# Kernel optimization log

Measured on AMD Instinct MI355X. Metric: run time of the kernel, lower is better.

Reference implementation:

```python
import jax, jax.numpy as jnp
import numpy as np

NEG_SLOPE = 0.2  # PyG GATConv default negative_slope


def _gat_conv(x, src, dst, W, a_src, a_dst, bias, heads, concat):
    """PyG-style GATConv (eval mode, self-loops already appended to src/dst).
    x: [N, Fin], W: [Fin, heads*C], a_src/a_dst: [heads, C], bias matches output.
    """
    N = x.shape[0]
    C = W.shape[1] // heads
    xw = (x @ W).reshape(N, heads, C)                      # [N, H, C]
    alpha_s = jnp.sum(xw * a_src, axis=-1)                 # [N, H]
    alpha_d = jnp.sum(xw * a_dst, axis=-1)                 # [N, H]
    e = jax.nn.leaky_relu(alpha_s[src] + alpha_d[dst], NEG_SLOPE)  # [E, H]
    # softmax over incoming edges of each destination node (numerically stable)
    m = jax.ops.segment_max(e, dst, num_segments=N)        # [N, H]
    e = jnp.exp(e - m[dst])
    denom = jax.ops.segment_sum(e, dst, num_segments=N)    # [N, H]
    alpha = e / denom[dst]                                 # [E, H]
    out = jax.ops.segment_sum(alpha[:, :, None] * xw[src], dst, num_segments=N)  # [N, H, C]
    if concat:
        out = out.reshape(N, heads * C)
    else:
        out = out.mean(axis=1)
    return out + bias


def setup_inputs() -> dict:
    key = jax.random.key(0)
    ks = jax.random.split(key, 10)
    N, E, FIN, FOUT, H1, C1 = 100000, 1600000, 128, 16, 4, 8
    x = jax.random.normal(ks[0], (N, FIN), jnp.float32)
    edge_index = jax.random.randint(ks[1], (2, E), 0, N, dtype=jnp.int32)
    W1 = jax.random.normal(ks[2], (FIN, H1 * C1), jnp.float32) / np.sqrt(FIN)
    a1_src = jax.random.normal(ks[3], (H1, C1), jnp.float32) / np.sqrt(C1)
    a1_dst = jax.random.normal(ks[4], (H1, C1), jnp.float32) / np.sqrt(C1)
    b1 = jnp.zeros((H1 * C1,), jnp.float32)
    W2 = jax.random.normal(ks[5], (H1 * C1, FOUT), jnp.float32) / np.sqrt(H1 * C1)
    a2_src = jax.random.normal(ks[6], (1, FOUT), jnp.float32) / np.sqrt(FOUT)
    a2_dst = jax.random.normal(ks[7], (1, FOUT), jnp.float32) / np.sqrt(FOUT)
    b2 = jnp.zeros((FOUT,), jnp.float32)
    return {"x": x, "edge_index": edge_index, "W1": W1, "a1_src": a1_src,
            "a1_dst": a1_dst, "b1": b1, "W2": W2, "a2_src": a2_src,
            "a2_dst": a2_dst, "b2": b2}


def reference(x, edge_index, W1, a1_src, a1_dst, b1, W2, a2_src, a2_dst, b2):
    N = x.shape[0]
    # PyG GATConv add_self_loops=True default
    loop = jnp.arange(N, dtype=edge_index.dtype)
    src = jnp.concatenate([edge_index[0], loop])
    dst = jnp.concatenate([edge_index[1], loop])
    # eval mode: F.dropout is identity
    h = _gat_conv(x, src, dst, W1, a1_src, a1_dst, b1, heads=4, concat=True)
    h = jax.nn.elu(h)
    h = _gat_conv(h, src, dst, W2, a2_src, a2_dst, b2, heads=1, concat=True)
    return jax.nn.log_softmax(h, axis=1)
```

## Files before the change

### kernel.cpp

```cpp
#include <hip/hip_runtime.h>
#include <math.h>

#define NN 100000
#define NE 1600000
#define ET (NE + NN)
#define FIN 128
#define H1 4
#define C1 8
#define F1 32
#define FOUT 16
#define NSLOPE 0.2f

#define PARTW 256
#define PSHIFT 8
#define NPART ((NN + PARTW - 1) / PARTW)
#define CHUNK 8192
#define NBLK ((ET + CHUNK - 1) / CHUNK)
#define CPAD 16
#define SMASK 0x1FFFF

typedef _Float16 half8 __attribute__((ext_vector_type(8)));
typedef _Float16 half2_t __attribute__((ext_vector_type(2)));
typedef float f32x4 __attribute__((ext_vector_type(4)));


__device__ inline int wave_incl_scan(int v) {
#pragma unroll
    for (int off = 1; off < 64; off <<= 1) {
        int u = __shfl_up(v, off);
        if ((threadIdx.x & 63) >= off) v += u;
    }
    return v;
}

__device__ inline int block_excl_scan(int v, int* wsum, int nw) {
    int t = threadIdx.x, wid = t >> 6, lane = t & 63;
    int incl = wave_incl_scan(v);
    if (lane == 63) wsum[wid] = incl;
    __syncthreads();
    if (wid == 0) {
        int wv = (lane < nw) ? wsum[lane] : 0;
        wv = wave_incl_scan(wv);
        if (lane < nw) wsum[lane] = wv;
    }
    __syncthreads();
    return incl - v + (wid ? wsum[wid - 1] : 0);
}


__global__ __launch_bounds__(1024) void k_hist(const int* __restrict__ dstA, int* __restrict__ ptotal) {
    __shared__ int h[NPART];
    int t = threadIdx.x;
    for (int i = t; i < NPART; i += 1024) h[i] = 0;
    __syncthreads();
    int base = blockIdx.x * CHUNK;
#pragma unroll
    for (int k = 0; k < CHUNK / 1024; k++) {
        int e = base + k * 1024 + t;
        if (e < ET) {
            int d = (e < NE) ? dstA[e] : (e - NE);
            atomicAdd(&h[d >> PSHIFT], 1);
        }
    }
    __syncthreads();
    for (int i = t; i < NPART; i += 1024)
        if (h[i]) atomicAdd(&ptotal[i * CPAD], h[i]);
}

__global__ __launch_bounds__(512) void k_pbase(const int* __restrict__ ptotal, int* __restrict__ pbase,
                                               int* __restrict__ gcur, int* __restrict__ rowstart) {
    __shared__ int wsum[8];
    int t = threadIdx.x;
    int v = (t < NPART) ? ptotal[t * CPAD] : 0;
    int excl = block_excl_scan(v, wsum, 8);
    if (t < NPART) { pbase[t] = excl; gcur[t * CPAD] = excl; }
    if (t == 0) { pbase[NPART] = ET; rowstart[NN] = ET; }
}

__global__ __launch_bounds__(1024) void k_part(const int* __restrict__ srcA, const int* __restrict__ dstA,
                                               int* __restrict__ gcur, int* __restrict__ pairs) {
    __shared__ int h[NPART];
    __shared__ int cur[NPART];
    int t = threadIdx.x;
    for (int i = t; i < NPART; i += 1024) h[i] = 0;
    __syncthreads();
    int base = blockIdx.x * CHUNK;
#pragma unroll
    for (int k = 0; k < CHUNK / 1024; k++) {
        int e = base + k * 1024 + t;
        if (e < ET) {
            int d = (e < NE) ? dstA[e] : (e - NE);
            atomicAdd(&h[d >> PSHIFT], 1);
        }
    }
    __syncthreads();
    for (int i = t; i < NPART; i += 1024) {
        int c = h[i];
        cur[i] = c ? atomicAdd(&gcur[i * CPAD], c) : 0;
    }
    __syncthreads();
#pragma unroll
    for (int k = 0; k < CHUNK / 1024; k++) {
        int e = base + k * 1024 + t;
        if (e < ET) {
            int s, d;
            if (e < NE) { s = srcA[e]; d = dstA[e]; }
            else        { s = e - NE;  d = s; }
            int pos = atomicAdd(&cur[d >> PSHIFT], 1);
            pairs[pos] = ((d & (PARTW - 1)) << 17) | s;
        }
    }
}

__global__ __launch_bounds__(1024) void k_sort(const int* __restrict__ pbase, const int* __restrict__ pairs,
                                               int* __restrict__ rowstart, int* __restrict__ epack) {
    __shared__ int hist[PARTW];
    __shared__ int sa[PARTW], sb[PARTW];
    int p = blockIdx.x;
    int t = threadIdx.x;
    int n0 = p << PSHIFT;
    int nn = min(PARTW, NN - n0);
    int base = pbase[p];
    int cnt = pbase[p + 1] - base;
    if (t < PARTW) hist[t] = 0;
    __syncthreads();
    for (int i = t; i < cnt; i += 1024)
        atomicAdd(&hist[pairs[base + i] >> 17], 1);
    __syncthreads();
    if (t < PARTW) sa[t] = hist[t];
    __syncthreads();
    int* pin = sa; int* pout = sb;
    for (int off = 1; off < PARTW; off <<= 1) {
        if (t < PARTW) pout[t] = pin[t] + ((t >= off) ? pin[t - off] : 0);
        __syncthreads();
        int* tmp = pin; pin = pout; pout = tmp;
    }
    int excl = 0;
    if (t < PARTW) {
        excl = pin[t] - hist[t];
        if (t < nn) rowstart[n0 + t] = base + excl;
    }
    __syncthreads();
    if (t < PARTW) hist[t] = excl;
    __syncthreads();
    for (int i = t; i < cnt; i += 1024) {
        int v = pairs[base + i];
        int pos = base + atomicAdd(&hist[v >> 17], 1);
        epack[pos] = v;
    }
}


__global__ __launch_bounds__(256) void k_gemm1(const float* __restrict__ x, const float* __restrict__ W1,
        const float* __restrict__ a1s, const float* __restrict__ a1d,
        _Float16* __restrict__ xw1h, float* __restrict__ as1, float* __restrict__ ad1) {
    __shared__ _Float16 w1t[F1 * FIN];
    __shared__ float xs[256 * F1];
    int t = threadIdx.x;
    {
        int i0 = t * 16;
#pragma unroll
        for (int i = 0; i < 16; i++) {
            int idx = i0 + i;
            int k = idx >> 5, n = idx & 31;
            w1t[n * FIN + k] = (_Float16)W1[idx];
        }
    }
    __syncthreads();
    int w = t >> 6, l = t & 63;
    int q = l >> 4, r16 = l & 15;
    int nblk = blockIdx.x * 256;
    int n0 = nblk + w * 64;
    half8 bf[4][2];
#pragma unroll
    for (int kc = 0; kc < 4; kc++)
#pragma unroll
        for (int nt = 0; nt < 2; nt++)
            bf[kc][nt] = *(const half8*)&w1t[(nt * 16 + r16) * FIN + kc * 32 + q * 8];
#pragma unroll
    for (int mt = 0; mt < 4; mt++) {
        int row = n0 + mt * 16 + r16;
        int rowc = min(row, NN - 1);
        const float4* xp = (const float4*)(x + (size_t)rowc * FIN + q * 8);
        half8 af[4];
#pragma unroll
        for (int kc = 0; kc < 4; kc++) {
            float4 u = xp[kc * 8];
            float4 v = xp[kc * 8 + 1];
            half8 a;
            a[0] = (_Float16)u.x; a[1] = (_Float16)u.y; a[2] = (_Float16)u.z; a[3] = (_Float16)u.w;
            a[4] = (_Float16)v.x; a[5] = (_Float16)v.y; a[6] = (_Float16)v.z; a[7] = (_Float16)v.w;
            af[kc] = a;
        }
        f32x4 acc0 = {0.f, 0.f, 0.f, 0.f};
        f32x4 acc1 = {0.f, 0.f, 0.f, 0.f};
#pragma unroll
        for (int kc = 0; kc < 4; kc++) {
            acc0 = __builtin_amdgcn_mfma_f32_16x16x32_f16(af[kc], bf[kc][0], acc0, 0, 0, 0);
            acc1 = __builtin_amdgcn_mfma_f32_16x16x32_f16(af[kc], bf[kc][1], acc1, 0, 0, 0);
        }
#pragma unroll
        for (int r = 0; r < 4; r++) {
            xs[(w * 64 + mt * 16 + q * 4 + r) * F1 + r16] = acc0[r];
            xs[(w * 64 + mt * 16 + q * 4 + r) * F1 + 16 + r16] = acc1[r];
        }
    }
    int node = nblk + w * 64 + l;
    if (node < NN) {
        const float4* xr = (const float4*)&xs[(w * 64 + l) * F1];
        float rowv[F1];
#pragma unroll
        for (int j = 0; j < 8; j++) {
            float4 v = xr[j];
            rowv[j * 4] = v.x; rowv[j * 4 + 1] = v.y; rowv[j * 4 + 2] = v.z; rowv[j * 4 + 3] = v.w;
        }
        half8* o8 = (half8*)(xw1h + (size_t)node * F1);
#pragma unroll
        for (int c8 = 0; c8 < F1 / 8; c8++) {
            half8 o;
#pragma unroll
            for (int k = 0; k < 8; k++) o[k] = (_Float16)rowv[c8 * 8 + k];
            o8[c8] = o;
        }
        float ss[H1], dd[H1];
#pragma unroll
        for (int h = 0; h < H1; h++) {
            ss[h] = 0.f; dd[h] = 0.f;
#pragma unroll
            for (int c = 0; c < C1; c++) {
                ss[h] = fmaf(rowv[h * C1 + c], a1s[h * C1 + c], ss[h]);
                dd[h] = fmaf(rowv[h * C1 + c], a1d[h * C1 + c], dd[h]);
            }
        }
        ((float4*)as1)[node] = make_float4(ss[0], ss[1], ss[2], ss[3]);
        ((float4*)ad1)[node] = make_float4(dd[0], dd[1], dd[2], dd[3]);
    }
}


__global__ __launch_bounds__(256) void k_gather1(const int* __restrict__ rowstart, const int* __restrict__ epack,
        const float* __restrict__ as1, const float* __restrict__ ad1,
        const _Float16* __restrict__ xw1h, const float* __restrict__ b1,
        _Float16* __restrict__ h1h) {
    int n = blockIdx.x * 4 + (threadIdx.x >> 6);
    if (n >= NN) return;
    int l = threadIdx.x & 63;
    int g = l >> 4;
    int j = l & 15;
    int h = j >> 2;
    float adh = ad1[n * H1 + h];
    const half2_t* xw = (const half2_t*)xw1h;
    int beg = rowstart[n], end = rowstart[n + 1];
    float a0 = 0.f, a1v = 0.f, ad = 0.f;
    int i = beg + g;
    for (; i + 4 < end; i += 8) {
        int s0 = epack[i] & SMASK, s1 = epack[i + 4] & SMASK;
        float e0 = as1[s0 * H1 + h] + adh;
        float e1 = as1[s1 * H1 + h] + adh;
        half2_t v0 = xw[s0 * 16 + j];
        half2_t v1 = xw[s1 * 16 + j];
        e0 = (e0 > 0.f) ? e0 : NSLOPE * e0;
        e1 = (e1 > 0.f) ? e1 : NSLOPE * e1;
        float w0 = __expf(e0), w1 = __expf(e1);
        ad += w0 + w1;
        a0  = fmaf(w0, (float)v0[0], fmaf(w1, (float)v1[0], a0));
        a1v = fmaf(w0, (float)v0[1], fmaf(w1, (float)v1[1], a1v));
    }
    for (; i < end; i += 4) {
        int s0 = epack[i] & SMASK;
        float e0 = as1[s0 * H1 + h] + adh;
        half2_t v0 = xw[s0 * 16 + j];
        e0 = (e0 > 0.f) ? e0 : NSLOPE * e0;
        float w0 = __expf(e0);
        ad += w0;
        a0  = fmaf(w0, (float)v0[0], a0);
        a1v = fmaf(w0, (float)v0[1], a1v);
    }
#pragma unroll
    for (int off = 16; off < 64; off <<= 1) {
        a0  += __shfl_xor(a0, off);
        a1v += __shfl_xor(a1v, off);
        ad  += __shfl_xor(ad, off);
    }
    float y0 = a0 / ad + b1[2 * j];
    float y1 = a1v / ad + b1[2 * j + 1];
    y0 = (y0 > 0.f) ? y0 : expm1f(y0);
    y1 = (y1 > 0.f) ? y1 : expm1f(y1);
    if (l < 16) {
        half2_t o; o[0] = (_Float16)y0; o[1] = (_Float16)y1;
        ((half2_t*)h1h)[(size_t)n * 16 + j] = o;
    }
}


__global__ __launch_bounds__(256) void k_node2(const _Float16* __restrict__ h1h, const float* __restrict__ W2,
        const float* __restrict__ a2s, const float* __restrict__ a2d,
        _Float16* __restrict__ xw2h, float* __restrict__ as2, float* __restrict__ ad2) {
    int n = blockIdx.x * 256 + threadIdx.x;
    if (n >= NN) return;
    float acc[FOUT];
#pragma unroll
    for (int j = 0; j < FOUT; j++) acc[j] = 0.f;
    const half8* h8 = (const half8*)(h1h + (size_t)n * F1);
#pragma unroll
    for (int i8 = 0; i8 < F1 / 8; i8++) {
        half8 hv = h8[i8];
#pragma unroll
        for (int kk = 0; kk < 8; kk++) {
            float hk = (float)hv[kk];
            int i = i8 * 8 + kk;
#pragma unroll
            for (int j = 0; j < FOUT; j++)
                acc[j] = fmaf(hk, W2[i * FOUT + j], acc[j]);
        }
    }
    float ss = 0.f, dd = 0.f;
#pragma unroll
    for (int j = 0; j < FOUT; j++) {
        ss = fmaf(acc[j], a2s[j], ss);
        dd = fmaf(acc[j], a2d[j], dd);
    }
    half8* o8 = (half8*)(xw2h + (size_t)n * FOUT);
#pragma unroll
    for (int j8 = 0; j8 < FOUT / 8; j8++) {
        half8 o;
#pragma unroll
        for (int k = 0; k < 8; k++) o[k] = (_Float16)acc[j8 * 8 + k];
        o8[j8] = o;
    }
    as2[n] = ss;
    ad2[n] = dd;
}


__global__ __launch_bounds__(256) void k_gather2(const int* __restrict__ rowstart, const int* __restrict__ epack,
        const float* __restrict__ as2, const float* __restrict__ ad2,
        const _Float16* __restrict__ xw2h, const float* __restrict__ b2,
        float* __restrict__ out) {
    int n = blockIdx.x * 4 + (threadIdx.x >> 6);
    if (n >= NN) return;
    int l = threadIdx.x & 63;
    int g = l >> 3;
    int j = l & 7;
    float adn = ad2[n];
    const half2_t* xw = (const half2_t*)xw2h;
    int beg = rowstart[n], end = rowstart[n + 1];
    float a0 = 0.f, a1v = 0.f, ad = 0.f;
    int i = beg + g;
    for (; i + 8 < end; i += 16) {
        int s0 = epack[i] & SMASK, s1 = epack[i + 8] & SMASK;
        float e0 = as2[s0] + adn;
        float e1 = as2[s1] + adn;
        half2_t v0 = xw[s0 * 8 + j];
        half2_t v1 = xw[s1 * 8 + j];
        e0 = (e0 > 0.f) ? e0 : NSLOPE * e0;
        e1 = (e1 > 0.f) ? e1 : NSLOPE * e1;
        float w0 = __expf(e0), w1 = __expf(e1);
        ad += w0 + w1;
        a0  = fmaf(w0, (float)v0[0], fmaf(w1, (float)v1[0], a0));
        a1v = fmaf(w0, (float)v0[1], fmaf(w1, (float)v1[1], a1v));
    }
    for (; i < end; i += 8) {
        int s0 = epack[i] & SMASK;
        float e0 = as2[s0] + adn;
        half2_t v0 = xw[s0 * 8 + j];
        e0 = (e0 > 0.f) ? e0 : NSLOPE * e0;
        float w0 = __expf(e0);
        ad += w0;
        a0  = fmaf(w0, (float)v0[0], a0);
        a1v = fmaf(w0, (float)v0[1], a1v);
    }
#pragma unroll
    for (int off = 8; off < 64; off <<= 1) {
        a0  += __shfl_xor(a0, off);
        a1v += __shfl_xor(a1v, off);
        ad  += __shfl_xor(ad, off);
    }
    float y0 = a0 / ad + b2[2 * j];
    float y1 = a1v / ad + b2[2 * j + 1];
    float m = fmaxf(y0, y1);
#pragma unroll
    for (int off = 1; off < 8; off <<= 1) m = fmaxf(m, __shfl_xor(m, off));
    float s = __expf(y0 - m) + __expf(y1 - m);
#pragma unroll
    for (int off = 1; off < 8; off <<= 1) s += __shfl_xor(s, off);
    float ls = logf(s);
    if (l < 8)
        ((float2*)out)[(size_t)n * 8 + j] = make_float2(y0 - m - ls, y1 - m - ls);
}


extern "C" void kernel_launch(void* const* d_in, const int* in_sizes, int n_in,
                              void* d_out, int out_size, void* d_ws, size_t ws_size,
                              hipStream_t stream) {
    const float* x   = (const float*)d_in[0];
    const int*   ei  = (const int*)d_in[1];
    const float* W1  = (const float*)d_in[2];
    const float* a1s = (const float*)d_in[3];
    const float* a1d = (const float*)d_in[4];
    const float* b1  = (const float*)d_in[5];
    const float* W2  = (const float*)d_in[6];
    const float* a2s = (const float*)d_in[7];
    const float* a2d = (const float*)d_in[8];
    const float* b2  = (const float*)d_in[9];
    float* out = (float*)d_out;

    const int* srcA = ei;
    const int* dstA = ei + NE;

    char* w = (char*)d_ws;
    size_t off = 0;
    auto carve = [&](size_t bytes) -> void* {
        void* p = w + off;
        off = (off + bytes + 255) & ~(size_t)255;
        return p;
    };
    _Float16* xw1h = (_Float16*)carve((size_t)NN * F1 * 2);
    float* as1     = (float*)carve((size_t)NN * H1 * 4);
    float* ad1     = (float*)carve((size_t)NN * H1 * 4);
    size_t h1_off  = off;
    _Float16* h1h  = (_Float16*)carve((size_t)NN * F1 * 2);
    _Float16* xw2h = (_Float16*)carve((size_t)NN * FOUT * 2);
    float* as2     = (float*)carve((size_t)NN * 4);
    float* ad2     = (float*)carve((size_t)NN * 4);
    int* pairs     = (int*)(w + h1_off);
    int* rowstart  = (int*)carve((size_t)(NN + 1) * 4);
    int* epack     = (int*)carve((size_t)ET * 4);
    int* ptotal    = (int*)carve((size_t)NPART * CPAD * 4);
    int* gcur      = (int*)carve((size_t)NPART * CPAD * 4);
    int* pbase     = (int*)carve((size_t)(NPART + 1) * 4);
    (void)ws_size; (void)in_sizes; (void)n_in; (void)out_size;

    hipMemsetAsync(ptotal, 0, (size_t)NPART * CPAD * 4, stream);

    k_hist  <<<NBLK, 1024, 0, stream>>>(dstA, ptotal);
    k_pbase <<<1, 512, 0, stream>>>(ptotal, pbase, gcur, rowstart);
    k_part  <<<NBLK, 1024, 0, stream>>>(srcA, dstA, gcur, pairs);
    k_sort  <<<NPART, 1024, 0, stream>>>(pbase, pairs, rowstart, epack);

    k_gemm1 <<<(NN + 255) / 256, 256, 0, stream>>>(x, W1, a1s, a1d, xw1h, as1, ad1);
    k_gather1<<<(NN + 3) / 4, 256, 0, stream>>>(rowstart, epack, as1, ad1, xw1h, b1, h1h);
    k_node2 <<<(NN + 255) / 256, 256, 0, stream>>>(h1h, W2, a2s, a2d, xw2h, as2, ad2);
    k_gather2<<<(NN + 3) / 4, 256, 0, stream>>>(rowstart, epack, as2, ad2, xw2h, b2, out);
}
```

Measured before the change: 245.6 us.

## Software-pipeline edge gathers and widen per-lane feature loads in GAT aggregation

Both gather kernels now prefetch the next pair of edge indices two iterations ahead and the source features one iteration ahead, so the dependent index-then-feature loads overlap across iterations. Indices are clamped to the row end to keep reads in bounds. Layer 1 also switches to 8 lanes per edge, each loading 4 halfs, so 8 edges run in parallel per wave instead of 4. Division is replaced by a reciprocal multiply. This adds register pressure and some redundant clamped loads on short rows.

```diff
diff --git a/kernel.cpp b/kernel.cpp
--- a/kernel.cpp
+++ b/kernel.cpp
@@ -20,6 +20,7 @@
 #define SMASK 0x1FFFF
 
 typedef _Float16 half8 __attribute__((ext_vector_type(8)));
+typedef _Float16 half4_t __attribute__((ext_vector_type(4)));
 typedef _Float16 half2_t __attribute__((ext_vector_type(2)));
 typedef float f32x4 __attribute__((ext_vector_type(4)));
 
@@ -245,50 +246,70 @@
     int n = blockIdx.x * 4 + (threadIdx.x >> 6);
     if (n >= NN) return;
     int l = threadIdx.x & 63;
-    int g = l >> 4;
-    int j = l & 15;
-    int h = j >> 2;
+    int g = l >> 3;
+    int j = l & 7;
+    int h = j >> 1;
     float adh = ad1[n * H1 + h];
-    const half2_t* xw = (const half2_t*)xw1h;
+    const half4_t* xw = (const half4_t*)xw1h;
     int beg = rowstart[n], end = rowstart[n + 1];
-    float a0 = 0.f, a1v = 0.f, ad = 0.f;
+    int endm1 = end - 1;
+    float a0 = 0.f, a1 = 0.f, a2 = 0.f, a3 = 0.f, ad = 0.f;
     int i = beg + g;
-    for (; i + 4 < end; i += 8) {
-        int s0 = epack[i] & SMASK, s1 = epack[i + 4] & SMASK;
-        float e0 = as1[s0 * H1 + h] + adh;
-        float e1 = as1[s1 * H1 + h] + adh;
-        half2_t v0 = xw[s0 * 16 + j];
-        half2_t v1 = xw[s1 * 16 + j];
+    int i0 = min(i, endm1), i1 = min(i + 8, endm1);
+    int c0 = epack[i0] & SMASK, c1 = epack[i1] & SMASK;
+    int i2 = min(i + 16, endm1), i3 = min(i + 24, endm1);
+    int sn0 = epack[i2] & SMASK, sn1 = epack[i3] & SMASK;
+    float f0 = as1[c0 * H1 + h], f1 = as1[c1 * H1 + h];
+    half4_t v0 = xw[c0 * 8 + j], v1 = xw[c1 * 8 + j];
+    while (i + 8 < end) {
+        float nf0 = as1[sn0 * H1 + h], nf1 = as1[sn1 * H1 + h];
+        half4_t nv0 = xw[sn0 * 8 + j], nv1 = xw[sn1 * 8 + j];
+        int p0 = min(i + 32, endm1), p1 = min(i + 40, endm1);
+        int u0 = epack[p0] & SMASK, u1 = epack[p1] & SMASK;
+        float e0 = f0 + adh, e1 = f1 + adh;
         e0 = (e0 > 0.f) ? e0 : NSLOPE * e0;
         e1 = (e1 > 0.f) ? e1 : NSLOPE * e1;
         float w0 = __expf(e0), w1 = __expf(e1);
         ad += w0 + w1;
-        a0  = fmaf(w0, (float)v0[0], fmaf(w1, (float)v1[0], a0));
-        a1v = fmaf(w0, (float)v0[1], fmaf(w1, (float)v1[1], a1v));
-    }
-    for (; i < end; i += 4) {
-        int s0 = epack[i] & SMASK;
-        float e0 = as1[s0 * H1 + h] + adh;
-        half2_t v0 = xw[s0 * 16 + j];
+        a0 = fmaf(w0, (float)v0[0], fmaf(w1, (float)v1[0], a0));
+        a1 = fmaf(w0, (float)v0[1], fmaf(w1, (float)v1[1], a1));
+        a2 = fmaf(w0, (float)v0[2], fmaf(w1, (float)v1[2], a2));
+        a3 = fmaf(w0, (float)v0[3], fmaf(w1, (float)v1[3], a3));
+        f0 = nf0; f1 = nf1; v0 = nv0; v1 = nv1;
+        sn0 = u0; sn1 = u1;
+        i += 16;
+    }
+    if (i < end) {
+        float e0 = f0 + adh;
         e0 = (e0 > 0.f) ? e0 : NSLOPE * e0;
         float w0 = __expf(e0);
         ad += w0;
-        a0  = fmaf(w0, (float)v0[0], a0);
-        a1v = fmaf(w0, (float)v0[1], a1v);
-    }
-#pragma unroll
-    for (int off = 16; off < 64; off <<= 1) {
-        a0  += __shfl_xor(a0, off);
-        a1v += __shfl_xor(a1v, off);
-        ad  += __shfl_xor(ad, off);
-    }
-    float y0 = a0 / ad + b1[2 * j];
-    float y1 = a1v / ad + b1[2 * j + 1];
-    y0 = (y0 > 0.f) ? y0 : expm1f(y0);
-    y1 = (y1 > 0.f) ? y1 : expm1f(y1);
-    if (l < 16) {
-        half2_t o; o[0] = (_Float16)y0; o[1] = (_Float16)y1;
-        ((half2_t*)h1h)[(size_t)n * 16 + j] = o;
+        a0 = fmaf(w0, (float)v0[0], a0);
+        a1 = fmaf(w0, (float)v0[1], a1);
+        a2 = fmaf(w0, (float)v0[2], a2);
+        a3 = fmaf(w0, (float)v0[3], a3);
+    }
+#pragma unroll
+    for (int off = 8; off < 64; off <<= 1) {
+        a0 += __shfl_xor(a0, off);
+        a1 += __shfl_xor(a1, off);
+        a2 += __shfl_xor(a2, off);
+        a3 += __shfl_xor(a3, off);
+        ad += __shfl_xor(ad, off);
+    }
+    if (l < 8) {
+        float inv = 1.0f / ad;
+        float y0 = fmaf(a0, inv, b1[4 * j]);
+        float y1 = fmaf(a1, inv, b1[4 * j + 1]);
+        float y2 = fmaf(a2, inv, b1[4 * j + 2]);
+        float y3 = fmaf(a3, inv, b1[4 * j + 3]);
+        y0 = (y0 > 0.f) ? y0 : expm1f(y0);
+        y1 = (y1 > 0.f) ? y1 : expm1f(y1);
+        y2 = (y2 > 0.f) ? y2 : expm1f(y2);
+        y3 = (y3 > 0.f) ? y3 : expm1f(y3);
+        half4_t o;
+        o[0] = (_Float16)y0; o[1] = (_Float16)y1; o[2] = (_Float16)y2; o[3] = (_Float16)y3;
+        ((half4_t*)h1h)[(size_t)n * 8 + j] = o;
     }
 }
 
@@ -345,25 +366,33 @@
     float adn = ad2[n];
     const half2_t* xw = (const half2_t*)xw2h;
     int beg = rowstart[n], end = rowstart[n + 1];
+    int endm1 = end - 1;
     float a0 = 0.f, a1v = 0.f, ad = 0.f;
     int i = beg + g;
-    for (; i + 8 < end; i += 16) {
-        int s0 = epack[i] & SMASK, s1 = epack[i + 8] & SMASK;
-        float e0 = as2[s0] + adn;
-        float e1 = as2[s1] + adn;
-        half2_t v0 = xw[s0 * 8 + j];
-        half2_t v1 = xw[s1 * 8 + j];
+    int i0 = min(i, endm1), i1 = min(i + 8, endm1);
+    int c0 = epack[i0] & SMASK, c1 = epack[i1] & SMASK;
+    int i2 = min(i + 16, endm1), i3 = min(i + 24, endm1);
+    int sn0 = epack[i2] & SMASK, sn1 = epack[i3] & SMASK;
+    float f0 = as2[c0], f1 = as2[c1];
+    half2_t v0 = xw[c0 * 8 + j], v1 = xw[c1 * 8 + j];
+    while (i + 8 < end) {
+        float nf0 = as2[sn0], nf1 = as2[sn1];
+        half2_t nv0 = xw[sn0 * 8 + j], nv1 = xw[sn1 * 8 + j];
+        int p0 = min(i + 32, endm1), p1 = min(i + 40, endm1);
+        int u0 = epack[p0] & SMASK, u1 = epack[p1] & SMASK;
+        float e0 = f0 + adn, e1 = f1 + adn;
         e0 = (e0 > 0.f) ? e0 : NSLOPE * e0;
         e1 = (e1 > 0.f) ? e1 : NSLOPE * e1;
         float w0 = __expf(e0), w1 = __expf(e1);
         ad += w0 + w1;
         a0  = fmaf(w0, (float)v0[0], fmaf(w1, (float)v1[0], a0));
         a1v = fmaf(w0, (float)v0[1], fmaf(w1, (float)v1[1], a1v));
-    }
-    for (; i < end; i += 8) {
-        int s0 = epack[i] & SMASK;
-        float e0 = as2[s0] + adn;
-        half2_t v0 = xw[s0 * 8 + j];
+        f0 = nf0; f1 = nf1; v0 = nv0; v1 = nv1;
+        sn0 = u0; sn1 = u1;
+        i += 16;
+    }
+    if (i < end) {
+        float e0 = f0 + adn;
         e0 = (e0 > 0.f) ? e0 : NSLOPE * e0;
         float w0 = __expf(e0);
         ad += w0;
@@ -376,8 +405,9 @@
         a1v += __shfl_xor(a1v, off);
         ad  += __shfl_xor(ad, off);
     }
-    float y0 = a0 / ad + b2[2 * j];
-    float y1 = a1v / ad + b2[2 * j + 1];
+    float inv = 1.0f / ad;
+    float y0 = fmaf(a0, inv, b2[2 * j]);
+    float y1 = fmaf(a1v, inv, b2[2 * j + 1]);
     float m = fmaxf(y0, y1);
 #pragma unroll
     for (int off = 1; off < 8; off <<= 1) m = fmaxf(m, __shfl_xor(m, off));
@@ -425,7 +455,7 @@
     float* ad2     = (float*)carve((size_t)NN * 4);
     int* pairs     = (int*)(w + h1_off);
     int* rowstart  = (int*)carve((size_t)(NN + 1) * 4);
-    int* epack     = (int*)carve((size_t)ET * 4);
+    int* epack     = (int*)carve((size_t)(ET + 64) * 4);
     int* ptotal    = (int*)carve((size_t)NPART * CPAD * 4);
     int* gcur      = (int*)carve((size_t)NPART * CPAD * 4);
     int* pbase     = (int*)carve((size_t)(NPART + 1) * 4);
```

Result: no change. 246.3 us (+0.3%).
